# Kernel tuning notes

Hardware: AMD Instinct MI355X
Metric: run time of the kernel (lower is better)

The kernel has to match this reference:

```python
import jax, jax.numpy as jnp
import numpy as np

B, W, N = 4, 8, 1024
F_IN, HID, OUT = 256, 256, 128


def setup_inputs() -> dict:
    key = jax.random.key(0)
    ks = jax.random.split(key, 8)
    X = jax.random.normal(ks[0], (B, W, N, F_IN), dtype=jnp.float32)
    adj = jax.random.uniform(ks[1], (B, W, N, N), dtype=jnp.float32)
    # Linear params, torch default init: U(-1/sqrt(fan_in), 1/sqrt(fan_in))
    def lin(k, fi, fo):
        k1, k2 = jax.random.split(k)
        bnd = 1.0 / np.sqrt(fi)
        Wm = jax.random.uniform(k1, (fi, fo), minval=-bnd, maxval=bnd, dtype=jnp.float32)
        bm = jax.random.uniform(k2, (fo,), minval=-bnd, maxval=bnd, dtype=jnp.float32)
        return Wm, bm
    W1, b1 = lin(ks[2], F_IN, HID)
    W2, b2 = lin(ks[3], HID, HID)
    W3, b3 = lin(ks[4], HID, OUT)
    return {"X": X, "adj": adj, "W1": W1, "b1": b1, "W2": W2, "b2": b2, "W3": W3, "b3": b3}


def _normalize(adj):
    # adj: [B, W, N, N]. adj_hat = adj + I; sym degree norm D^-1/2 A D^-1/2
    n = adj.shape[-1]
    adj_hat = adj + jnp.eye(n, dtype=adj.dtype)
    d = jnp.sum(adj_hat, axis=-1) ** (-0.5)            # [B, W, N]
    # diag(d) @ adj_hat @ diag(d) == row/col scaling (same math, no N^3 diag matmuls)
    return adj_hat * d[..., :, None] * d[..., None, :]


def reference(X, adj, W1, b1, W2, b2, W3, b3):
    adj_norm = _normalize(adj)                          # [B, W, N, N]
    h = X
    for Wm, bm in ((W1, b1), (W2, b2), (W3, b3)):
        h = jnp.einsum('bwnm,bwmf->bwnf', adj_norm, h)  # aggregate
        h = jax.nn.relu(jnp.einsum('bwnf,fo->bwno', h, Wm) + bm)
    return h                                            # [B, W, N, OUT]
```

## Files before the change

kernel.cpp:

```cpp
#include <hip/hip_runtime.h>
#include <hip/hip_bf16.h>
#include <cstdint>
#include <cstddef>

#define NN 1024
#define FF 256

typedef __attribute__((ext_vector_type(8))) short bf16x8;
typedef __attribute__((ext_vector_type(4))) float f32x4;

typedef __attribute__((address_space(1))) const void* gas_ptr;
typedef __attribute__((address_space(3))) void* las_ptr;

__device__ __forceinline__ short f2bf(float x) {
  unsigned int u = __float_as_uint(x);
  u = (u + 0x7fffu + ((u >> 16) & 1u)) >> 16;
  return (short)u;
}


__global__ __launch_bounds__(256)
void dinv_cast(const float* __restrict__ adj, float* __restrict__ dinv,
               short* __restrict__ Ahat) {
  __shared__ float wsum[64];
  int b = blockIdx.x;
  int bw = b >> 6, s = b & 63;
  int t = threadIdx.x;
  int wid = t >> 6, lane = t & 63;
  int row = lane & 15;
  int rloc = (s << 4) + row;
  int kg = (lane >> 4) & 3;
  const float* arow = adj + ((size_t)(bw << 10) + rloc) * NN;
  short* outb = Ahat + ((size_t)bw << 20) + ((size_t)s << 14) + (t << 3);
  float ssum = 0.f;
  #pragma unroll
  for (int it = 0; it < 8; it++) {
    int col = (it << 7) + (wid << 5) + (kg << 3);
    float4 a0 = *(const float4*)(arow + col);
    float4 a1 = *(const float4*)(arow + col + 4);
    float v[8] = {a0.x, a0.y, a0.z, a0.w, a1.x, a1.y, a1.z, a1.w};
    union { ushort o[8]; int4 q; } pk;
    #pragma unroll
    for (int j = 0; j < 8; j++) {
      v[j] += (rloc == col + j) ? 1.f : 0.f;
      ssum += v[j];
      pk.o[j] = (ushort)f2bf(v[j]);
    }
    *(int4*)(outb + (it << 11)) = pk.q;
  }
  ssum += __shfl_down(ssum, 32, 64);
  ssum += __shfl_down(ssum, 16, 64);
  if (lane < 16) wsum[(wid << 4) + lane] = ssum;
  __syncthreads();
  if (t < 16) {
    float tot = wsum[t] + wsum[16 + t] + wsum[32 + t] + wsum[48 + t];
    dinv[(bw << 10) + (s << 4) + t] = rsqrtf(tot);
  }
}

__global__ __launch_bounds__(256)
void transpose_x(const float* __restrict__ X, const float* __restrict__ dinv,
                 short* __restrict__ XT) {
  __shared__ short T[64][72];
  int bwo = blockIdx.z;
  int n0 = blockIdx.x << 6, f0 = blockIdx.y << 6;
  int t = threadIdx.x;
  {
    int n = t >> 2, fc = (t & 3) << 4;
    float dn = dinv[(bwo << 10) + n0 + n];
    const float* src = X + (((size_t)bwo * NN + n0 + n) * FF) + f0 + fc;
    #pragma unroll
    for (int i = 0; i < 4; i++) {
      float4 v = ((const float4*)src)[i];
      ushort4 p;
      p.x = (unsigned short)f2bf(v.x * dn); p.y = (unsigned short)f2bf(v.y * dn);
      p.z = (unsigned short)f2bf(v.z * dn); p.w = (unsigned short)f2bf(v.w * dn);
      *(ushort4*)&T[n][fc + (i << 2)] = p;
    }
  }
  __syncthreads();
  {
    int f = t >> 2, nc = (t & 3) << 4;
    int fg = f0 + f, ng = n0 + nc;
    short tmp[16];
    #pragma unroll
    for (int i = 0; i < 16; i++) tmp[i] = T[nc + i][f];
    size_t e0 = ((size_t)bwo << 18) + ((size_t)(fg >> 4) << 14) + ((ng >> 5) << 9)
              + (((ng & 31) >> 3) << 7) + ((fg & 15) << 3);
    *(int4*)(XT + e0)       = *(int4*)&tmp[0];
    *(int4*)(XT + e0 + 128) = *(int4*)&tmp[8];
  }
}

__global__ __launch_bounds__(256)
void transpose_w3(const float* __restrict__ W1, const float* __restrict__ W2,
                  const float* __restrict__ W3,
                  short* __restrict__ T1, short* __restrict__ T2,
                  short* __restrict__ T3) {
  int idx = blockIdx.x * 256 + threadIdx.x;
  const float* W; short* T; int FO; int loc;
  if (idx < 65536)       { W = W1; T = T1; FO = 256; loc = idx; }
  else if (idx < 131072) { W = W2; T = T2; FO = 256; loc = idx - 65536; }
  else                   { W = W3; T = T3; FO = 128; loc = idx - 131072; }
  int fo = loc >> 8, fi = loc & 255;
  if (fo >= FO) return;
  size_t e = (size_t)((fo >> 4) << 12) + ((fi >> 5) << 9)
           + (((fi & 31) >> 3) << 7) + ((fo & 15) << 3) + (fi & 7);
  T[e] = f2bf(W[fi * FO + fo]);
}

template<int F_OUT, bool FINAL>
__global__ __launch_bounds__(512)
void gcn_layer(const short* __restrict__ Ahat,
               const float* __restrict__ dinv,
               const short* __restrict__ Gin,
               const short* __restrict__ WT,
               const float* __restrict__ bias,
               short* __restrict__ Gout,
               float* __restrict__ Out) {
  __shared__ __align__(16) short lds[49152];

  int b = blockIdx.x;
  int x = b & 7, m = b >> 3;
  int bw = (x << 2) + (m >> 3);
  int rb = m & 7;
  int r0 = rb << 7;

  int tid = threadIdx.x;
  int wid = tid >> 6, lane = tid & 63;
  int l15 = lane & 15, l4 = lane >> 4;
  int wr = wid >> 2, wf = wid & 3;

  const float* dvB = dinv + (bw << 10);
  const short* Abase = Ahat + ((size_t)bw << 20) + ((size_t)(rb << 3) << 14);
  const short* Hbase = Gin  + ((size_t)bw << 18);

  auto stage = [&](int sel, int t) {
    char* base = (char*)lds + sel * 49152;
    int kb = t << 1;
    #pragma unroll
    for (int i = 0; i < 2; i++) {
      int slot = (i << 9) + tid;
      int c = slot >> 6, o = slot & 63;
      const short* g = Abase + ((size_t)(c >> 1) << 14) + ((size_t)(kb + (c & 1)) << 9) + (o << 3);
      __builtin_amdgcn_global_load_lds((gas_ptr)g, (las_ptr)(base + (slot << 4)), 16, 0, 0);
    }
    #pragma unroll
    for (int i = 0; i < 4; i++) {
      int slot = (i << 9) + tid;
      int c = slot >> 6, o = slot & 63;
      const short* g = Hbase + ((size_t)(c >> 1) << 14) + ((size_t)(kb + (c & 1)) << 9) + (o << 3);
      __builtin_amdgcn_global_load_lds((gas_ptr)g, (las_ptr)(base + 16384 + (slot << 4)), 16, 0, 0);
    }
  };

  f32x4 acc[4][4];
  #pragma unroll
  for (int ah = 0; ah < 4; ah++)
    #pragma unroll
    for (int aa = 0; aa < 4; aa++) acc[ah][aa] = f32x4{0.f, 0.f, 0.f, 0.f};

  stage(0, 0);
  asm volatile("s_waitcnt vmcnt(0)" ::: "memory");
  __builtin_amdgcn_s_barrier();

  for (int t = 0; t < 16; ++t) {
    if (t < 15) stage((t + 1) & 1, t + 1);
    const char* base = (const char*)lds + (t & 1) * 49152;
    bf16x8 a[4][2], h[4][2];
    #pragma unroll
    for (int aa = 0; aa < 4; aa++) {
      int c = ((wr << 2) + aa) << 1;
      a[aa][0] = *(const bf16x8*)(base + (c << 10) + (lane << 4));
      a[aa][1] = *(const bf16x8*)(base + ((c + 1) << 10) + (lane << 4));
    }
    #pragma unroll
    for (int ah = 0; ah < 4; ah++) {
      int c = ((wf << 2) + ah) << 1;
      h[ah][0] = *(const bf16x8*)(base + 16384 + (c << 10) + (lane << 4));
      h[ah][1] = *(const bf16x8*)(base + 16384 + ((c + 1) << 10) + (lane << 4));
    }
    __builtin_amdgcn_s_setprio(1);
    #pragma unroll
    for (int kt = 0; kt < 2; kt++)
      #pragma unroll
      for (int ah = 0; ah < 4; ah++)
        #pragma unroll
        for (int aa = 0; aa < 4; aa++)
          acc[ah][aa] = __builtin_amdgcn_mfma_f32_16x16x32_bf16(
              h[ah][kt], a[aa][kt], acc[ah][aa], 0, 0, 0);
    __builtin_amdgcn_s_setprio(0);
    asm volatile("s_waitcnt vmcnt(0)" ::: "memory");
    __builtin_amdgcn_sched_barrier(0);
    __builtin_amdgcn_s_barrier();
  }

  short* aggL = lds;
  float dsc[4];
  #pragma unroll
  for (int aa = 0; aa < 4; aa++) dsc[aa] = dvB[r0 + (wr << 6) + (aa << 4) + l15];
  #pragma unroll
  for (int ah = 0; ah < 4; ah++)
    #pragma unroll
    for (int aa = 0; aa < 4; aa++) {
      int r = (wr << 6) + (aa << 4) + l15;
      int fB = ((wf << 6) + (ah << 4) + (l4 << 2)) << 1;
      int off = (r * 544 + (fB ^ ((r & 7) << 4))) >> 1;
      ushort4 p;
      p.x = (unsigned short)f2bf(acc[ah][aa][0] * dsc[aa]);
      p.y = (unsigned short)f2bf(acc[ah][aa][1] * dsc[aa]);
      p.z = (unsigned short)f2bf(acc[ah][aa][2] * dsc[aa]);
      p.w = (unsigned short)f2bf(acc[ah][aa][3] * dsc[aa]);
      *(ushort4*)(aggL + off) = p;
    }
  __syncthreads();

  constexpr int NFO = F_OUT / 64;
  const short* Wbase = WT + (size_t)(wf * NFO) * 4096 + (lane << 3);
  f32x4 acc2[4][NFO];
  #pragma unroll
  for (int am = 0; am < 4; am++)
    #pragma unroll
    for (int nf = 0; nf < NFO; nf++) acc2[am][nf] = f32x4{0.f, 0.f, 0.f, 0.f};

  #pragma unroll
  for (int kt = 0; kt < 8; kt++) {
    bf16x8 af[4];
    #pragma unroll
    for (int am = 0; am < 4; am++) {
      int r = (wr << 6) + (am << 4) + l15;
      int fB = (kt << 6) + (l4 << 4);
      af[am] = *(const bf16x8*)(aggL + ((r * 544 + (fB ^ ((r & 7) << 4))) >> 1));
    }
    #pragma unroll
    for (int nf = 0; nf < NFO; nf++) {
      bf16x8 wv = *(const bf16x8*)(Wbase + (size_t)nf * 4096 + (kt << 9));
      #pragma unroll
      for (int am = 0; am < 4; am++)
        acc2[am][nf] = __builtin_amdgcn_mfma_f32_16x16x32_bf16(af[am], wv, acc2[am][nf], 0, 0, 0);
    }
  }

  #pragma unroll
  for (int am = 0; am < 4; am++) {
    int nodeLoc = (wr << 6) + (am << 4) + (l4 << 2);
    float4 dn4 = *(const float4*)(dvB + r0 + nodeLoc);
    float dn[4] = {dn4.x, dn4.y, dn4.z, dn4.w};
    #pragma unroll
    for (int nf = 0; nf < NFO; nf++) {
      int fo = wf * (F_OUT / 4) + (nf << 4) + l15;
      float bb = bias[fo];
      float v[4];
      #pragma unroll
      for (int j = 0; j < 4; j++) v[j] = fmaxf(acc2[am][nf][j] + bb, 0.f);
      if (!FINAL) {
        ushort4 p;
        p.x = (unsigned short)f2bf(v[0] * dn[0]);
        p.y = (unsigned short)f2bf(v[1] * dn[1]);
        p.z = (unsigned short)f2bf(v[2] * dn[2]);
        p.w = (unsigned short)f2bf(v[3] * dn[3]);
        size_t e = (size_t)bw * (F_OUT * 1024) + ((size_t)(fo >> 4) << 14)
                 + ((size_t)((rb << 2) + (wr << 1) + (am >> 1)) << 9)
                 + ((size_t)(((am & 1) << 1) + (l4 >> 1)) << 7)
                 + ((fo & 15) << 3) + ((l4 & 1) << 2);
        *(ushort4*)(Gout + e) = p;
      } else {
        float* ob = Out + ((size_t)(bw << 10) + r0 + nodeLoc) * F_OUT + fo;
        ob[0]         = v[0];
        ob[F_OUT]     = v[1];
        ob[2 * F_OUT] = v[2];
        ob[3 * F_OUT] = v[3];
      }
    }
  }
}

extern "C" void kernel_launch(void* const* d_in, const int* in_sizes, int n_in,
                              void* d_out, int out_size, void* d_ws, size_t ws_size,
                              hipStream_t stream) {
  const float* X   = (const float*)d_in[0];
  const float* adj = (const float*)d_in[1];
  const float* W1  = (const float*)d_in[2];
  const float* b1  = (const float*)d_in[3];
  const float* W2  = (const float*)d_in[4];
  const float* b2  = (const float*)d_in[5];
  const float* W3  = (const float*)d_in[6];
  const float* b3  = (const float*)d_in[7];
  float* out = (float*)d_out;

  char* ws = (char*)d_ws;
  float* dinv = (float*)ws;
  short* WT1  = (short*)(ws + 131072);
  short* WT2  = (short*)(ws + 262144);
  short* WT3  = (short*)(ws + 393216);
  short* bufA = (short*)(ws + 458752);
  short* bufB = (short*)(ws + 458752 + 16777216);
  short* Ahat = (short*)(ws + 458752 + 2 * 16777216);

  dinv_cast<<<2048, 256, 0, stream>>>(adj, dinv, Ahat);
  transpose_w3<<<640, 256, 0, stream>>>(W1, W2, W3, WT1, WT2, WT3);
  transpose_x<<<dim3(16, 4, 32), 256, 0, stream>>>(X, dinv, bufA);

  gcn_layer<256, false><<<256, 512, 0, stream>>>(Ahat, dinv, bufA, WT1, b1, bufB, nullptr);
  gcn_layer<256, false><<<256, 512, 0, stream>>>(Ahat, dinv, bufB, WT2, b2, bufA, nullptr);
  gcn_layer<128, true ><<<256, 512, 0, stream>>>(Ahat, dinv, bufA, WT3, b3, nullptr, out);
}
```

Measured before the change: 133.4 us.

## Triple-buffer GCN aggregation pipeline and merge X/W preprocessing kernels

The aggregation loop in gcn_layer moves from double to triple buffering in LDS (96KB to 144KB). Loads are issued two stages ahead in half-stage chunks, and each k-step is split into two sub-steps with partial vmcnt waits, so global loads overlap more MFMA work. The X transpose and weight transpose kernels are merged into one launch to save a kernel launch. The larger LDS footprint limits blocks per CU, and the extra barriers per iteration add sync cost.

```diff
diff --git a/kernel.cpp b/kernel.cpp
--- a/kernel.cpp
+++ b/kernel.cpp
@@ -59,54 +59,56 @@
 }
 
 __global__ __launch_bounds__(256)
-void transpose_x(const float* __restrict__ X, const float* __restrict__ dinv,
-                 short* __restrict__ XT) {
+void preproc_xw(const float* __restrict__ X, const float* __restrict__ dinv,
+                short* __restrict__ XT,
+                const float* __restrict__ W1, const float* __restrict__ W2,
+                const float* __restrict__ W3,
+                short* __restrict__ T1, short* __restrict__ T2,
+                short* __restrict__ T3) {
   __shared__ short T[64][72];
-  int bwo = blockIdx.z;
-  int n0 = blockIdx.x << 6, f0 = blockIdx.y << 6;
+  int b = blockIdx.x;
   int t = threadIdx.x;
-  {
-    int n = t >> 2, fc = (t & 3) << 4;
-    float dn = dinv[(bwo << 10) + n0 + n];
-    const float* src = X + (((size_t)bwo * NN + n0 + n) * FF) + f0 + fc;
-    #pragma unroll
-    for (int i = 0; i < 4; i++) {
-      float4 v = ((const float4*)src)[i];
-      ushort4 p;
-      p.x = (unsigned short)f2bf(v.x * dn); p.y = (unsigned short)f2bf(v.y * dn);
-      p.z = (unsigned short)f2bf(v.z * dn); p.w = (unsigned short)f2bf(v.w * dn);
-      *(ushort4*)&T[n][fc + (i << 2)] = p;
-    }
-  }
-  __syncthreads();
-  {
-    int f = t >> 2, nc = (t & 3) << 4;
-    int fg = f0 + f, ng = n0 + nc;
-    short tmp[16];
-    #pragma unroll
-    for (int i = 0; i < 16; i++) tmp[i] = T[nc + i][f];
-    size_t e0 = ((size_t)bwo << 18) + ((size_t)(fg >> 4) << 14) + ((ng >> 5) << 9)
-              + (((ng & 31) >> 3) << 7) + ((fg & 15) << 3);
-    *(int4*)(XT + e0)       = *(int4*)&tmp[0];
-    *(int4*)(XT + e0 + 128) = *(int4*)&tmp[8];
-  }
-}
-
-__global__ __launch_bounds__(256)
-void transpose_w3(const float* __restrict__ W1, const float* __restrict__ W2,
-                  const float* __restrict__ W3,
-                  short* __restrict__ T1, short* __restrict__ T2,
-                  short* __restrict__ T3) {
-  int idx = blockIdx.x * 256 + threadIdx.x;
-  const float* W; short* T; int FO; int loc;
-  if (idx < 65536)       { W = W1; T = T1; FO = 256; loc = idx; }
-  else if (idx < 131072) { W = W2; T = T2; FO = 256; loc = idx - 65536; }
-  else                   { W = W3; T = T3; FO = 128; loc = idx - 131072; }
-  int fo = loc >> 8, fi = loc & 255;
-  if (fo >= FO) return;
-  size_t e = (size_t)((fo >> 4) << 12) + ((fi >> 5) << 9)
-           + (((fi & 31) >> 3) << 7) + ((fo & 15) << 3) + (fi & 7);
-  T[e] = f2bf(W[fi * FO + fo]);
+  if (b < 2048) {
+    int bwo = b >> 6;
+    int n0 = (b & 15) << 6, f0 = ((b >> 4) & 3) << 6;
+    {
+      int n = t >> 2, fc = (t & 3) << 4;
+      float dn = dinv[(bwo << 10) + n0 + n];
+      const float* src = X + (((size_t)bwo * NN + n0 + n) * FF) + f0 + fc;
+      #pragma unroll
+      for (int i = 0; i < 4; i++) {
+        float4 v = ((const float4*)src)[i];
+        ushort4 p;
+        p.x = (unsigned short)f2bf(v.x * dn); p.y = (unsigned short)f2bf(v.y * dn);
+        p.z = (unsigned short)f2bf(v.z * dn); p.w = (unsigned short)f2bf(v.w * dn);
+        *(ushort4*)&T[n][fc + (i << 2)] = p;
+      }
+    }
+    __syncthreads();
+    {
+      int f = t >> 2, nc = (t & 3) << 4;
+      int fg = f0 + f, ng = n0 + nc;
+      short tmp[16];
+      #pragma unroll
+      for (int i = 0; i < 16; i++) tmp[i] = T[nc + i][f];
+      size_t e0 = ((size_t)bwo << 18) + ((size_t)(fg >> 4) << 14) + ((ng >> 5) << 9)
+                + (((ng & 31) >> 3) << 7) + ((fg & 15) << 3);
+      *(int4*)(XT + e0)       = *(int4*)&tmp[0];
+      *(int4*)(XT + e0 + 128) = *(int4*)&tmp[8];
+    }
+  } else {
+    int idx = (b - 2048) * 256 + t;
+    const float* W; short* Td; int FO; int loc;
+    if (idx < 65536)       { W = W1; Td = T1; FO = 256; loc = idx; }
+    else if (idx < 131072) { W = W2; Td = T2; FO = 256; loc = idx - 65536; }
+    else                   { W = W3; Td = T3; FO = 128; loc = idx - 131072; }
+    int fo = loc >> 8, fi = loc & 255;
+    if (fo < FO) {
+      size_t e = (size_t)((fo >> 4) << 12) + ((fi >> 5) << 9)
+               + (((fi & 31) >> 3) << 7) + ((fo & 15) << 3) + (fi & 7);
+      Td[e] = f2bf(W[fi * FO + fo]);
+    }
+  }
 }
 
 template<int F_OUT, bool FINAL>
@@ -118,7 +120,7 @@
                const float* __restrict__ bias,
                short* __restrict__ Gout,
                float* __restrict__ Out) {
-  __shared__ __align__(16) short lds[49152];
+  __shared__ __align__(16) short lds[73728];
 
   int b = blockIdx.x;
   int x = b & 7, m = b >> 3;
@@ -133,25 +135,26 @@
 
   const float* dvB = dinv + (bw << 10);
   const short* Abase = Ahat + ((size_t)bw << 20) + ((size_t)(rb << 3) << 14);
-  const short* Hbase = Gin  + ((size_t)bw << 18);
-
-  auto stage = [&](int sel, int t) {
+  const short* Hbase = Gin + ((size_t)bw << 18);
+
+  auto stage3 = [&](int sel, int t, int half) {
     char* base = (char*)lds + sel * 49152;
     int kb = t << 1;
     #pragma unroll
-    for (int i = 0; i < 2; i++) {
-      int slot = (i << 9) + tid;
-      int c = slot >> 6, o = slot & 63;
-      const short* g = Abase + ((size_t)(c >> 1) << 14) + ((size_t)(kb + (c & 1)) << 9) + (o << 3);
+    for (int i = 0; i < 3; i++) {
+      int j = half * 3 + i;
+      int slot = (j << 9) + tid;
+      const short* g;
+      if (j < 2) {
+        int c = slot >> 6, o = slot & 63;
+        g = Abase + ((size_t)(c >> 1) << 14) + ((size_t)(kb + (c & 1)) << 9) + (o << 3);
+      } else {
+        int s2 = slot - 1024;
+        int c = s2 >> 6, o = s2 & 63;
+        g = Hbase + ((size_t)(c >> 1) << 14) + ((size_t)(kb + (c & 1)) << 9) + (o << 3);
+      }
       __builtin_amdgcn_global_load_lds((gas_ptr)g, (las_ptr)(base + (slot << 4)), 16, 0, 0);
     }
-    #pragma unroll
-    for (int i = 0; i < 4; i++) {
-      int slot = (i << 9) + tid;
-      int c = slot >> 6, o = slot & 63;
-      const short* g = Hbase + ((size_t)(c >> 1) << 14) + ((size_t)(kb + (c & 1)) << 9) + (o << 3);
-      __builtin_amdgcn_global_load_lds((gas_ptr)g, (las_ptr)(base + 16384 + (slot << 4)), 16, 0, 0);
-    }
   };
 
   f32x4 acc[4][4];
@@ -160,39 +163,49 @@
     #pragma unroll
     for (int aa = 0; aa < 4; aa++) acc[ah][aa] = f32x4{0.f, 0.f, 0.f, 0.f};
 
-  stage(0, 0);
-  asm volatile("s_waitcnt vmcnt(0)" ::: "memory");
+  stage3(0, 0, 0); stage3(0, 0, 1);
+  stage3(1, 1, 0); stage3(1, 1, 1);
+  asm volatile("s_waitcnt vmcnt(6)" ::: "memory");
+  __builtin_amdgcn_sched_barrier(0);
   __builtin_amdgcn_s_barrier();
 
+  #pragma unroll
   for (int t = 0; t < 16; ++t) {
-    if (t < 15) stage((t + 1) & 1, t + 1);
-    const char* base = (const char*)lds + (t & 1) * 49152;
-    bf16x8 a[4][2], h[4][2];
-    #pragma unroll
-    for (int aa = 0; aa < 4; aa++) {
-      int c = ((wr << 2) + aa) << 1;
-      a[aa][0] = *(const bf16x8*)(base + (c << 10) + (lane << 4));
-      a[aa][1] = *(const bf16x8*)(base + ((c + 1) << 10) + (lane << 4));
-    }
-    #pragma unroll
-    for (int ah = 0; ah < 4; ah++) {
-      int c = ((wf << 2) + ah) << 1;
-      h[ah][0] = *(const bf16x8*)(base + 16384 + (c << 10) + (lane << 4));
-      h[ah][1] = *(const bf16x8*)(base + 16384 + ((c + 1) << 10) + (lane << 4));
-    }
-    __builtin_amdgcn_s_setprio(1);
-    #pragma unroll
-    for (int kt = 0; kt < 2; kt++)
+    const char* base = (const char*)lds + (t % 3) * 49152;
+    #pragma unroll
+    for (int p = 0; p < 2; ++p) {
+      if (t <= 13) stage3((t + 2) % 3, t + 2, p);
+      bf16x8 aT[4], hT[4];
+      #pragma unroll
+      for (int aa = 0; aa < 4; aa++) {
+        int c = (((wr << 2) + aa) << 1) + p;
+        aT[aa] = *(const bf16x8*)(base + (c << 10) + (lane << 4));
+      }
+      #pragma unroll
+      for (int ah = 0; ah < 4; ah++) {
+        int c = (((wf << 2) + ah) << 1) + p;
+        hT[ah] = *(const bf16x8*)(base + 16384 + (c << 10) + (lane << 4));
+      }
+      __builtin_amdgcn_s_barrier();
+      asm volatile("s_waitcnt lgkmcnt(0)" ::: "memory");
+      __builtin_amdgcn_sched_barrier(0);
+      __builtin_amdgcn_s_setprio(1);
       #pragma unroll
       for (int ah = 0; ah < 4; ah++)
         #pragma unroll
         for (int aa = 0; aa < 4; aa++)
           acc[ah][aa] = __builtin_amdgcn_mfma_f32_16x16x32_bf16(
-              h[ah][kt], a[aa][kt], acc[ah][aa], 0, 0, 0);
-    __builtin_amdgcn_s_setprio(0);
-    asm volatile("s_waitcnt vmcnt(0)" ::: "memory");
-    __builtin_amdgcn_sched_barrier(0);
-    __builtin_amdgcn_s_barrier();
+              hT[ah], aT[aa], acc[ah][aa], 0, 0, 0);
+      __builtin_amdgcn_s_setprio(0);
+      if (p == 1 && t <= 13) {
+        asm volatile("s_waitcnt vmcnt(6)" ::: "memory");
+        __builtin_amdgcn_sched_barrier(0);
+      } else if (p == 1 && t == 14) {
+        asm volatile("s_waitcnt vmcnt(0)" ::: "memory");
+        __builtin_amdgcn_sched_barrier(0);
+      }
+      __builtin_amdgcn_s_barrier();
+    }
   }
 
   short* aggL = lds;
@@ -298,8 +311,7 @@
   short* Ahat = (short*)(ws + 458752 + 2 * 16777216);
 
   dinv_cast<<<2048, 256, 0, stream>>>(adj, dinv, Ahat);
-  transpose_w3<<<640, 256, 0, stream>>>(W1, W2, W3, WT1, WT2, WT3);
-  transpose_x<<<dim3(16, 4, 32), 256, 0, stream>>>(X, dinv, bufA);
+  preproc_xw<<<2688, 256, 0, stream>>>(X, dinv, bufA, W1, W2, W3, WT1, WT2, WT3);
 
   gcn_layer<256, false><<<256, 512, 0, stream>>>(Ahat, dinv, bufA, WT1, b1, bufB, nullptr);
   gcn_layer<256, false><<<256, 512, 0, stream>>>(Ahat, dinv, bufB, WT2, b2, bufA, nullptr);
```

Measured after the change: 130.7 us. 1.02x faster.
